# Kernel tuning notes

Measured on AMD Instinct MI355X. Metric: run time of the kernel, lower is better.

Reference implementation:

```python
import jax, jax.numpy as jnp
import numpy as np

B, C, O, H, W = 16, 256, 256, 64, 64
T_DIM, E, K = 512, 4, 3


def setup_inputs() -> dict:
    key = jax.random.key(0)
    ks = jax.random.split(key, 12)
    def rn(k, shape, s=0.02):
        return jax.random.normal(k, shape, jnp.float32) * s
    return dict(
        x=jax.random.normal(ks[0], (B, C, H, W), jnp.float32),
        time_emb=jax.random.normal(ks[1], (B, T_DIM), jnp.float32),
        Wq=rn(ks[2], (C, T_DIM)), bq=jnp.zeros((C,), jnp.float32),
        Wk=rn(ks[3], (C, C)), bk=jnp.zeros((C,), jnp.float32),
        Wv=rn(ks[4], (C, C)), bv=jnp.zeros((C,), jnp.float32),
        Wm1=rn(ks[5], (C // 4, C)), bm1=jnp.zeros((C // 4,), jnp.float32),
        Wm2=rn(ks[6], (C, C // 4)), bm2=jnp.zeros((C,), jnp.float32),
        Wc=rn(ks[7], (E, C)), bc=jnp.zeros((E,), jnp.float32),
        expert_w=rn(ks[8], (E, O, C, K, K), s=0.05),  # [E, O, C_in/groups, K, K]
        expert_b=rn(ks[9], (E, O), s=0.05),
    )


def reference(x, time_emb, Wq, bq, Wk, bk, Wv, bv, Wm1, bm1, Wm2, bm2, Wc, bc, expert_w, expert_b):
    # --- router (eval mode: no gating noise) ---
    pooled = x.mean(axis=(2, 3))                      # [B, C] == avg_pool over full HxW
    q = time_emb @ Wq.T + bq                          # [B, C]
    k = pooled @ Wk.T + bk                            # [B, C]
    attn = jax.nn.sigmoid(q * k)
    v = pooled @ Wv.T + bv
    x_att = v * attn
    h = jax.nn.gelu(x_att @ Wm1.T + bm1, approximate=False) @ Wm2.T + bm2
    x_mix = x_att + h
    logits = x_mix @ Wc.T + bc                        # [B, E]
    rw = jnp.tanh(logits)                             # routing weights [B, E]

    # --- per-sample expert-weight mixing ---
    w_eff = jnp.einsum('be,eoihw->boihw', rw, expert_w)  # [B, O, C, K, K]
    b_eff = rw @ expert_b                                 # [B, O]

    # --- per-sample conv (equivalent to groups=B trick) ---
    def conv_one(xb, wb):
        # xb: [C, H, W], wb: [O, C, K, K]
        return jax.lax.conv_general_dilated(
            xb[None], wb, window_strides=(1, 1), padding=[(1, 1), (1, 1)],
            dimension_numbers=('NCHW', 'OIHW', 'NCHW'))[0]

    out = jax.vmap(conv_one)(x, w_eff)                 # [B, O, H, W]
    return out + b_eff[:, :, None, None]
```

## Files before the change

### kernel.cpp

```cpp
#include <hip/hip_runtime.h>

typedef __bf16 bf16x8 __attribute__((ext_vector_type(8)));
typedef float f32x4 __attribute__((ext_vector_type(4)));

__device__ __forceinline__ unsigned short f2bf(float f) {
  union { float f; unsigned int u; } v;
  v.f = f;
  unsigned int r = v.u + 0x7FFFu + ((v.u >> 16) & 1u);
  return (unsigned short)(r >> 16);
}

__device__ __forceinline__ void load_lds16(const void* g, void* l) {
  __builtin_amdgcn_global_load_lds(
      (__attribute__((address_space(1))) void*)(void*)g,
      (__attribute__((address_space(3))) void*)l, 16, 0, 0);
}

__global__ void transpose_kernel(const float* __restrict__ x, unsigned short* __restrict__ xTpad,
                                 float* __restrict__ part) {
  int bid = blockIdx.x;
  int b = bid / 66, hp = bid % 66;
  unsigned short* rowbase = xTpad + ((size_t)(b * 66 + hp)) * 66 * 256;
  int t = threadIdx.x;
  if (hp == 0 || hp == 65) {
    uint4 z = make_uint4(0u, 0u, 0u, 0u);
    for (int i = t; i < 2112; i += 256) ((uint4*)rowbase)[i] = z;
    return;
  }
  int h = hp - 1;
  __shared__ unsigned short lds[64][264];
  __shared__ float psum[256];
  const float* xb = x + ((size_t)b * 256 * 64 + h) * 64;
  int lane = t & 63;
  #pragma unroll
  for (int g = 0; g < 16; ++g) {
    int c = g * 16 + (t >> 4);
    int w0 = (t & 15) * 4;
    float4 v = *(const float4*)&xb[(size_t)c * 4096 + w0];
    lds[w0 + 0][c] = f2bf(v.x);
    lds[w0 + 1][c] = f2bf(v.y);
    lds[w0 + 2][c] = f2bf(v.z);
    lds[w0 + 3][c] = f2bf(v.w);
    float s = v.x + v.y + v.z + v.w;
    s += __shfl_xor(s, 1); s += __shfl_xor(s, 2);
    s += __shfl_xor(s, 4); s += __shfl_xor(s, 8);
    if ((lane & 15) == 0) psum[c] = s;
  }
  __syncthreads();
  #pragma unroll
  for (int p = 0; p < 8; ++p) {
    int w = p * 8 + (t >> 5);
    int seg = t & 31;
    uint4 u = *(const uint4*)&lds[w][seg * 8];
    *(uint4*)&rowbase[(w + 1) * 256 + seg * 8] = u;
  }
  if (t < 64) {
    uint4 z = make_uint4(0u, 0u, 0u, 0u);
    int row = (t >> 5) ? 65 : 0;
    *(uint4*)&rowbase[row * 256 + (t & 31) * 8] = z;
  }
  if (t < 256) part[((size_t)b * 64 + h) * 256 + t] = psum[t];
}

__global__ void router_kernel(
    const float* __restrict__ time_emb, const float* __restrict__ part,
    const float* __restrict__ Wq, const float* __restrict__ bq,
    const float* __restrict__ Wk, const float* __restrict__ bk,
    const float* __restrict__ Wv, const float* __restrict__ bv,
    const float* __restrict__ Wm1, const float* __restrict__ bm1,
    const float* __restrict__ Wm2, const float* __restrict__ bm2,
    const float* __restrict__ Wc, const float* __restrict__ bc,
    const float* __restrict__ expert_b,
    float* __restrict__ rw_out, float* __restrict__ beff_out) {
  int b = blockIdx.x, tid = threadIdx.x;
  int t = tid & 255;
  __shared__ float te[512], pl[256], qs[256], xa[256], m1s[64], xms[256], rws[4];
  te[tid] = time_emb[b * 512 + tid];
  if (tid < 256) {
    float s = 0.f;
    const float* pp = part + (size_t)b * 16384 + tid;
    for (int hh = 0; hh < 64; ++hh) s += pp[hh * 256];
    pl[tid] = s * (1.0f / 4096.0f);
  }
  __syncthreads();
  if (tid < 256) {
    float q = bq[t];
    const float4* wq4 = (const float4*)(Wq + (size_t)t * 512);
    #pragma unroll 4
    for (int i = 0; i < 128; ++i) {
      float4 w4 = wq4[i];
      q += w4.x * te[i*4] + w4.y * te[i*4+1] + w4.z * te[i*4+2] + w4.w * te[i*4+3];
    }
    qs[t] = q;
  } else {
    float k = bk[t], v = bv[t];
    const float4* wk4 = (const float4*)(Wk + (size_t)t * 256);
    const float4* wv4 = (const float4*)(Wv + (size_t)t * 256);
    #pragma unroll 4
    for (int i = 0; i < 64; ++i) {
      float4 a4 = wk4[i], b4 = wv4[i];
      float p0 = pl[i*4], p1 = pl[i*4+1], p2 = pl[i*4+2], p3 = pl[i*4+3];
      k += a4.x * p0 + a4.y * p1 + a4.z * p2 + a4.w * p3;
      v += b4.x * p0 + b4.y * p1 + b4.z * p2 + b4.w * p3;
    }
    xa[t] = k;
    xms[t] = v;
  }
  __syncthreads();
  if (tid < 256) {
    float k = xa[t], v = xms[t];
    float attn = 1.0f / (1.0f + expf(-(qs[t] * k)));
    float xatt = v * attn;
    qs[t] = xatt;
  }
  __syncthreads();
  if (tid < 64) {
    float s = bm1[tid];
    const float4* w1 = (const float4*)(Wm1 + (size_t)tid * 256);
    #pragma unroll 4
    for (int i = 0; i < 64; ++i) {
      float4 w4 = w1[i];
      s += w4.x * qs[i*4] + w4.y * qs[i*4+1] + w4.z * qs[i*4+2] + w4.w * qs[i*4+3];
    }
    m1s[tid] = 0.5f * s * (1.0f + erff(s * 0.7071067811865476f));
  }
  __syncthreads();
  if (tid < 256) {
    float hsum = bm2[t];
    const float* w2 = Wm2 + (size_t)t * 64;
    for (int j = 0; j < 64; ++j) hsum += m1s[j] * w2[j];
    xms[t] = qs[t] + hsum;
  }
  __syncthreads();
  if (tid < 4) {
    float s = bc[tid];
    const float* wc = Wc + (size_t)tid * 256;
    for (int i = 0; i < 256; ++i) s += xms[i] * wc[i];
    float r = tanhf(s);
    rws[tid] = r;
    rw_out[b * 4 + tid] = r;
  }
  __syncthreads();
  if (tid < 256) {
    float be = 0.f;
    #pragma unroll
    for (int e = 0; e < 4; ++e) be += rws[e] * expert_b[e * 256 + t];
    beff_out[b * 256 + t] = be;
  }
}

__global__ void wmix_kernel(const float* __restrict__ ew, const float* __restrict__ rw,
                            unsigned short* __restrict__ wmix) {
  int o = blockIdx.x, t = threadIdx.x;
  __shared__ float lew[4][2304];
  __shared__ float rsh[64];
  if (t < 64) rsh[t] = rw[t];
  #pragma unroll
  for (int e = 0; e < 4; ++e) {
    const float* s = ew + ((size_t)e * 256 + o) * 2304;
    #pragma unroll
    for (int j = 0; j < 9; ++j) lew[e][j * 256 + t] = s[j * 256 + t];
  }
  __syncthreads();
  float wv[4][9];
  #pragma unroll
  for (int e = 0; e < 4; ++e)
    #pragma unroll
    for (int tt = 0; tt < 9; ++tt) wv[e][tt] = lew[e][t * 9 + tt];
  for (int b = 0; b < 16; ++b) {
    float r0 = rsh[b*4], r1 = rsh[b*4+1], r2 = rsh[b*4+2], r3 = rsh[b*4+3];
    unsigned short* wo = wmix + ((size_t)b * 256 + o) * 2304 + t;
    #pragma unroll
    for (int tt = 0; tt < 9; ++tt) {
      float m = r0 * wv[0][tt] + r1 * wv[1][tt] + r2 * wv[2][tt] + r3 * wv[3][tt];
      wo[tt * 256] = f2bf(m);
    }
  }
}

__global__ __launch_bounds__(512, 2) void conv_kernel(
    const unsigned short* __restrict__ xT, const unsigned short* __restrict__ wmix,
    const float* __restrict__ beff, float* __restrict__ out) {
  __shared__ unsigned short As[2][16384];
  __shared__ unsigned short Bs[2][16384];
  int bid = blockIdx.x;
  int b = ((bid & 7) << 1) | ((bid >> 7) & 1);
  int nt = (bid >> 3) & 15;
  int h0 = nt << 2;
  int tid = threadIdx.x;
  int wid = tid >> 6, lane = tid & 63;
  int lm = lane & 15, lg = lane >> 4;
  int wm = wid >> 1, wn = wid & 1;

  const unsigned short* wmb = wmix + (size_t)b * 256 * 2304;
  const unsigned short* xTb = xT + (size_t)b * 66 * 66 * 256;

  int lr = lane >> 3;
  int slot_g = (lane & 7) ^ lr;
  int a_lane = lr * 2304 + slot_g * 8;
  int b_lane = lr * 256 + slot_g * 8;

  int sw0 = ((0 + lg) ^ (lm & 7)) * 8;
  int sw1 = ((4 + lg) ^ (lm & 7)) * 8;

  auto stA = [&](int buf, int s, int u) {
    const unsigned short* src = wmb + (size_t)(u * 64 + wid * 8) * 2304 + s * 64 + a_lane;
    load_lds16(src, &As[buf][(u * 64 + wid * 8) * 64]);
  };
  auto stB = [&](int buf, int s, int bh, int rq) {
    int tap = s >> 2;
    int kh = tap / 3, kw = tap - kh * 3;
    int c0 = (s & 3) * 64;
    const unsigned short* src =
        xTb + (size_t)((h0 + bh * 2 + rq + kh) * 66 + wid * 8 + kw) * 256 + c0 + b_lane;
    load_lds16(src, &Bs[buf][(bh * 128 + rq * 64 + wid * 8) * 64]);
  };

  f32x4 acc[4][8];
  #pragma unroll
  for (int mf = 0; mf < 4; ++mf)
    #pragma unroll
    for (int nf = 0; nf < 8; ++nf)
      acc[mf][nf] = (f32x4){0.f, 0.f, 0.f, 0.f};

  stA(0, 0, 0); stA(0, 0, 1); stA(0, 0, 2); stA(0, 0, 3);
  stB(0, 0, 0, 0); stB(0, 0, 1, 0);
  stB(0, 0, 0, 1); stB(0, 0, 1, 1);
  asm volatile("s_waitcnt vmcnt(2)" ::: "memory");
  __builtin_amdgcn_s_barrier();

  auto do_tile = [&](int t, int BUF) __attribute__((always_inline)) {
    bool st = (t < 35);
    int s = t + 1;
    bf16x8 a01[2][2], a23[2][2], bA[4][2], bB[4][2];
    #pragma unroll
    for (int mf = 0; mf < 2; ++mf) {
      a01[mf][0] = *(const bf16x8*)&As[BUF][(wm * 64 + mf * 16 + lm) * 64 + sw0];
      a01[mf][1] = *(const bf16x8*)&As[BUF][(wm * 64 + mf * 16 + lm) * 64 + sw1];
    }
    #pragma unroll
    for (int nf = 0; nf < 4; ++nf) {
      bA[nf][0] = *(const bf16x8*)&Bs[BUF][(wn * 128 + nf * 16 + lm) * 64 + sw0];
      bA[nf][1] = *(const bf16x8*)&Bs[BUF][(wn * 128 + nf * 16 + lm) * 64 + sw1];
    }
    if (st) {
      stA(BUF ^ 1, s, 0); stA(BUF ^ 1, s, 1); stA(BUF ^ 1, s, 2); stA(BUF ^ 1, s, 3);
      stB(BUF ^ 1, s, 0, 0); stB(BUF ^ 1, s, 1, 0);
      stB(BUF ^ 1, s, 0, 1); stB(BUF ^ 1, s, 1, 1);
    }
    __builtin_amdgcn_s_barrier();
    asm volatile("s_waitcnt lgkmcnt(0)" ::: "memory");
    __builtin_amdgcn_sched_barrier(0);
    __builtin_amdgcn_s_setprio(1);
    #pragma unroll
    for (int mf = 0; mf < 2; ++mf)
      #pragma unroll
      for (int nf = 0; nf < 4; ++nf)
        #pragma unroll
        for (int kk = 0; kk < 2; ++kk)
          acc[mf][nf] = __builtin_amdgcn_mfma_f32_16x16x32_bf16(a01[mf][kk], bA[nf][kk], acc[mf][nf], 0, 0, 0);
    __builtin_amdgcn_s_setprio(0);
    __builtin_amdgcn_s_barrier();
    #pragma unroll
    for (int mf = 0; mf < 2; ++mf) {
      a23[mf][0] = *(const bf16x8*)&As[BUF][(wm * 64 + (mf + 2) * 16 + lm) * 64 + sw0];
      a23[mf][1] = *(const bf16x8*)&As[BUF][(wm * 64 + (mf + 2) * 16 + lm) * 64 + sw1];
    }
    if (st) { asm volatile("s_waitcnt vmcnt(8)" ::: "memory"); }
    else    { asm volatile("s_waitcnt vmcnt(0)" ::: "memory"); }
    __builtin_amdgcn_s_barrier();
    asm volatile("s_waitcnt lgkmcnt(0)" ::: "memory");
    __builtin_amdgcn_sched_barrier(0);
    __builtin_amdgcn_s_setprio(1);
    #pragma unroll
    for (int mf = 0; mf < 2; ++mf)
      #pragma unroll
      for (int nf = 0; nf < 4; ++nf)
        #pragma unroll
        for (int kk = 0; kk < 2; ++kk)
          acc[mf + 2][nf] = __builtin_amdgcn_mfma_f32_16x16x32_bf16(a23[mf][kk], bA[nf][kk], acc[mf + 2][nf], 0, 0, 0);
    __builtin_amdgcn_s_setprio(0);
    __builtin_amdgcn_s_barrier();
    #pragma unroll
    for (int nf = 0; nf < 4; ++nf) {
      bB[nf][0] = *(const bf16x8*)&Bs[BUF][(wn * 128 + 64 + nf * 16 + lm) * 64 + sw0];
      bB[nf][1] = *(const bf16x8*)&Bs[BUF][(wn * 128 + 64 + nf * 16 + lm) * 64 + sw1];
    }
    __builtin_amdgcn_s_barrier();
    asm volatile("s_waitcnt lgkmcnt(0)" ::: "memory");
    __builtin_amdgcn_sched_barrier(0);
    __builtin_amdgcn_s_setprio(1);
    #pragma unroll
    for (int mf = 0; mf < 2; ++mf)
      #pragma unroll
      for (int nf = 0; nf < 4; ++nf)
        #pragma unroll
        for (int kk = 0; kk < 2; ++kk)
          acc[mf + 2][nf + 4] = __builtin_amdgcn_mfma_f32_16x16x32_bf16(a23[mf][kk], bB[nf][kk], acc[mf + 2][nf + 4], 0, 0, 0);
    __builtin_amdgcn_s_setprio(0);
    __builtin_amdgcn_s_barrier();
    __builtin_amdgcn_s_setprio(1);
    #pragma unroll
    for (int mf = 0; mf < 2; ++mf)
      #pragma unroll
      for (int nf = 0; nf < 4; ++nf)
        #pragma unroll
        for (int kk = 0; kk < 2; ++kk)
          acc[mf][nf + 4] = __builtin_amdgcn_mfma_f32_16x16x32_bf16(a01[mf][kk], bB[nf][kk], acc[mf][nf + 4], 0, 0, 0);
    __builtin_amdgcn_s_setprio(0);
    if (st) { asm volatile("s_waitcnt vmcnt(2)" ::: "memory"); }
    else    { asm volatile("s_waitcnt vmcnt(0)" ::: "memory"); }
    __builtin_amdgcn_s_barrier();
  };

  for (int th = 0; th < 18; ++th) {
    do_tile(2 * th, 0);
    do_tile(2 * th + 1, 1);
  }

  #pragma unroll
  for (int mf = 0; mf < 4; ++mf) {
    int o = wm * 64 + mf * 16 + lg * 4;
    float be0 = beff[b * 256 + o + 0];
    float be1 = beff[b * 256 + o + 1];
    float be2 = beff[b * 256 + o + 2];
    float be3 = beff[b * 256 + o + 3];
    #pragma unroll
    for (int nf = 0; nf < 8; ++nf) {
      int n = wn * 128 + nf * 16 + lm;
      int hh = h0 + (n >> 6), w = n & 63;
      float* op = out + (((size_t)(b * 256 + o)) * 64 + hh) * 64 + w;
      op[0]            = acc[mf][nf][0] + be0;
      op[4096]         = acc[mf][nf][1] + be1;
      op[2 * 4096]     = acc[mf][nf][2] + be2;
      op[3 * 4096]     = acc[mf][nf][3] + be3;
    }
  }
}

extern "C" void kernel_launch(void* const* d_in, const int* in_sizes, int n_in,
                              void* d_out, int out_size, void* d_ws, size_t ws_size,
                              hipStream_t stream) {
  const float* x        = (const float*)d_in[0];
  const float* time_emb = (const float*)d_in[1];
  const float* Wq = (const float*)d_in[2];
  const float* bq = (const float*)d_in[3];
  const float* Wk = (const float*)d_in[4];
  const float* bk = (const float*)d_in[5];
  const float* Wv = (const float*)d_in[6];
  const float* bv = (const float*)d_in[7];
  const float* Wm1 = (const float*)d_in[8];
  const float* bm1 = (const float*)d_in[9];
  const float* Wm2 = (const float*)d_in[10];
  const float* bm2 = (const float*)d_in[11];
  const float* Wc = (const float*)d_in[12];
  const float* bc = (const float*)d_in[13];
  const float* expert_w = (const float*)d_in[14];
  const float* expert_b = (const float*)d_in[15];
  float* out = (float*)d_out;

  char* ws = (char*)d_ws;
  float* rw   = (float*)(ws + 0);
  float* beff = (float*)(ws + 1024);
  float* part = (float*)(ws + 20480);
  unsigned short* xTpad = (unsigned short*)(ws + 1069056);
  unsigned short* wmix  = (unsigned short*)(ws + 1069056 + 35684352);

  transpose_kernel<<<1056, 256, 0, stream>>>(x, xTpad, part);
  router_kernel<<<16, 512, 0, stream>>>(time_emb, part, Wq, bq, Wk, bk, Wv, bv,
                                        Wm1, bm1, Wm2, bm2, Wc, bc, expert_b, rw, beff);
  wmix_kernel<<<256, 256, 0, stream>>>(expert_w, rw, wmix);
  conv_kernel<<<256, 512, 0, stream>>>(xTpad, wmix, beff, out);
}
```

Baseline: 152.6 us.

## Split conv LDS into quarter slots and stagger loads across MFMA phases

```diff
diff --git a/kernel.cpp b/kernel.cpp
--- a/kernel.cpp
+++ b/kernel.cpp
@@ -110,8 +110,7 @@
   if (tid < 256) {
     float k = xa[t], v = xms[t];
     float attn = 1.0f / (1.0f + expf(-(qs[t] * k)));
-    float xatt = v * attn;
-    qs[t] = xatt;
+    qs[t] = v * attn;
   }
   __syncthreads();
   if (tid < 64) {
@@ -181,8 +180,8 @@
 __global__ __launch_bounds__(512, 2) void conv_kernel(
     const unsigned short* __restrict__ xT, const unsigned short* __restrict__ wmix,
     const float* __restrict__ beff, float* __restrict__ out) {
-  __shared__ unsigned short As[2][16384];
-  __shared__ unsigned short Bs[2][16384];
+  __shared__ unsigned short As[4][8192];
+  __shared__ unsigned short Bs[4][8192];
   int bid = blockIdx.x;
   int b = ((bid & 7) << 1) | ((bid >> 7) & 1);
   int nt = (bid >> 3) & 15;
@@ -203,17 +202,15 @@
   int sw0 = ((0 + lg) ^ (lm & 7)) * 8;
   int sw1 = ((4 + lg) ^ (lm & 7)) * 8;
 
-  auto stA = [&](int buf, int s, int u) {
-    const unsigned short* src = wmb + (size_t)(u * 64 + wid * 8) * 2304 + s * 64 + a_lane;
-    load_lds16(src, &As[buf][(u * 64 + wid * 8) * 64]);
+  auto stA = [&](int slot, int kh, int cc, int kw, int u) {
+    const unsigned short* src =
+        wmb + (size_t)(u * 64 + wid * 8) * 2304 + (kh * 3 + kw) * 256 + cc * 64 + a_lane;
+    load_lds16(src, &As[slot][((u & 1) * 64 + wid * 8) * 64]);
   };
-  auto stB = [&](int buf, int s, int bh, int rq) {
-    int tap = s >> 2;
-    int kh = tap / 3, kw = tap - kh * 3;
-    int c0 = (s & 3) * 64;
+  auto stB = [&](int slot, int kh, int cc, int kw, int hg) {
     const unsigned short* src =
-        xTb + (size_t)((h0 + bh * 2 + rq + kh) * 66 + wid * 8 + kw) * 256 + c0 + b_lane;
-    load_lds16(src, &Bs[buf][(bh * 128 + rq * 64 + wid * 8) * 64]);
+        xTb + (size_t)((h0 + hg + kh) * 66 + wid * 8 + kw) * 256 + cc * 64 + b_lane;
+    load_lds16(src, &Bs[slot][((hg & 1) * 64 + wid * 8) * 64]);
   };
 
   f32x4 acc[4][8];
@@ -223,99 +220,182 @@
     for (int nf = 0; nf < 8; ++nf)
       acc[mf][nf] = (f32x4){0.f, 0.f, 0.f, 0.f};
 
-  stA(0, 0, 0); stA(0, 0, 1); stA(0, 0, 2); stA(0, 0, 3);
-  stB(0, 0, 0, 0); stB(0, 0, 1, 0);
-  stB(0, 0, 0, 1); stB(0, 0, 1, 1);
-  asm volatile("s_waitcnt vmcnt(2)" ::: "memory");
+  const int arow = (wm & 1) * 64;
+  const int aslot = wm >> 1;
+  const int bslot = wn;
+
+  stA(0, 0, 0, 0, 0); stA(0, 0, 0, 0, 1); stA(1, 0, 0, 0, 2); stA(1, 0, 0, 0, 3);
+  stB(0, 0, 0, 0, 0); stB(0, 0, 0, 0, 1); stB(1, 0, 0, 0, 2); stB(1, 0, 0, 0, 3);
+  stA(2, 0, 0, 1, 0); stA(2, 0, 0, 1, 1); stA(3, 0, 0, 1, 2); stA(3, 0, 0, 1, 3);
+  stB(2, 0, 0, 1, 0); stB(2, 0, 0, 1, 1); stB(3, 0, 0, 1, 2); stB(3, 0, 0, 1, 3);
+  asm volatile("s_waitcnt vmcnt(8)" ::: "memory");
   __builtin_amdgcn_s_barrier();
 
-  auto do_tile = [&](int t, int BUF) __attribute__((always_inline)) {
-    bool st = (t < 35);
-    int s = t + 1;
+  for (int i = 0; i < 18; ++i) {
+    bool st = (i < 17);
+    int ta = 2 * i + 2, tb = 2 * i + 3;
+    int kha = ta / 12, ra = ta % 12;
+    int cca = ra / 3,  kwa = ra % 3;
+    int khb = tb / 12, rb = tb % 12;
+    int ccb = rb / 3,  kwb = rb % 3;
+
     bf16x8 a01[2][2], a23[2][2], bA[4][2], bB[4][2];
+
     #pragma unroll
     for (int mf = 0; mf < 2; ++mf) {
-      a01[mf][0] = *(const bf16x8*)&As[BUF][(wm * 64 + mf * 16 + lm) * 64 + sw0];
-      a01[mf][1] = *(const bf16x8*)&As[BUF][(wm * 64 + mf * 16 + lm) * 64 + sw1];
+      a01[mf][0] = *(const bf16x8*)&As[aslot][(arow + mf * 16 + lm) * 64 + sw0];
+      a01[mf][1] = *(const bf16x8*)&As[aslot][(arow + mf * 16 + lm) * 64 + sw1];
     }
     #pragma unroll
     for (int nf = 0; nf < 4; ++nf) {
-      bA[nf][0] = *(const bf16x8*)&Bs[BUF][(wn * 128 + nf * 16 + lm) * 64 + sw0];
-      bA[nf][1] = *(const bf16x8*)&Bs[BUF][(wn * 128 + nf * 16 + lm) * 64 + sw1];
+      bA[nf][0] = *(const bf16x8*)&Bs[bslot][(nf * 16 + lm) * 64 + sw0];
+      bA[nf][1] = *(const bf16x8*)&Bs[bslot][(nf * 16 + lm) * 64 + sw1];
+    }
+    __builtin_amdgcn_s_barrier();
+    asm volatile("s_waitcnt lgkmcnt(0)" ::: "memory");
+    __builtin_amdgcn_sched_barrier(0);
+    __builtin_amdgcn_s_setprio(1);
+    #pragma unroll
+    for (int mf = 0; mf < 2; ++mf)
+      #pragma unroll
+      for (int nf = 0; nf < 4; ++nf)
+        #pragma unroll
+        for (int kk = 0; kk < 2; ++kk)
+          acc[mf][nf] = __builtin_amdgcn_mfma_f32_16x16x32_bf16(a01[mf][kk], bA[nf][kk], acc[mf][nf], 0, 0, 0);
+    __builtin_amdgcn_s_setprio(0);
+    __builtin_amdgcn_s_barrier();
+    #pragma unroll
+    for (int mf = 0; mf < 2; ++mf) {
+      a23[mf][0] = *(const bf16x8*)&As[aslot][(arow + (mf + 2) * 16 + lm) * 64 + sw0];
+      a23[mf][1] = *(const bf16x8*)&As[aslot][(arow + (mf + 2) * 16 + lm) * 64 + sw1];
+    }
+    __builtin_amdgcn_s_barrier();
+    asm volatile("s_waitcnt lgkmcnt(0)" ::: "memory");
+    __builtin_amdgcn_sched_barrier(0);
+    __builtin_amdgcn_s_setprio(1);
+    #pragma unroll
+    for (int mf = 0; mf < 2; ++mf)
+      #pragma unroll
+      for (int nf = 0; nf < 4; ++nf)
+        #pragma unroll
+        for (int kk = 0; kk < 2; ++kk)
+          acc[mf + 2][nf] = __builtin_amdgcn_mfma_f32_16x16x32_bf16(a23[mf][kk], bA[nf][kk], acc[mf + 2][nf], 0, 0, 0);
+    __builtin_amdgcn_s_setprio(0);
+    __builtin_amdgcn_s_barrier();
+    #pragma unroll
+    for (int nf = 0; nf < 4; ++nf) {
+      bB[nf][0] = *(const bf16x8*)&Bs[bslot][(64 + nf * 16 + lm) * 64 + sw0];
+      bB[nf][1] = *(const bf16x8*)&Bs[bslot][(64 + nf * 16 + lm) * 64 + sw1];
+    }
+    if (st) { stA(0, kha, cca, kwa, 0); stA(0, kha, cca, kwa, 1); }
+    __builtin_amdgcn_s_barrier();
+    asm volatile("s_waitcnt lgkmcnt(0)" ::: "memory");
+    __builtin_amdgcn_sched_barrier(0);
+    __builtin_amdgcn_s_setprio(1);
+    #pragma unroll
+    for (int mf = 0; mf < 2; ++mf)
+      #pragma unroll
+      for (int nf = 0; nf < 4; ++nf)
+        #pragma unroll
+        for (int kk = 0; kk < 2; ++kk)
+          acc[mf + 2][nf + 4] = __builtin_amdgcn_mfma_f32_16x16x32_bf16(a23[mf][kk], bB[nf][kk], acc[mf + 2][nf + 4], 0, 0, 0);
+    __builtin_amdgcn_s_setprio(0);
+    __builtin_amdgcn_s_barrier();
+    if (st) { stA(1, kha, cca, kwa, 2); stA(1, kha, cca, kwa, 3); }
+    __builtin_amdgcn_s_setprio(1);
+    #pragma unroll
+    for (int mf = 0; mf < 2; ++mf)
+      #pragma unroll
+      for (int nf = 0; nf < 4; ++nf)
+        #pragma unroll
+        for (int kk = 0; kk < 2; ++kk)
+          acc[mf][nf + 4] = __builtin_amdgcn_mfma_f32_16x16x32_bf16(a01[mf][kk], bB[nf][kk], acc[mf][nf + 4], 0, 0, 0);
+    __builtin_amdgcn_s_setprio(0);
+    if (st) { asm volatile("s_waitcnt vmcnt(4)" ::: "memory"); }
+    else    { asm volatile("s_waitcnt vmcnt(0)" ::: "memory"); }
+    __builtin_amdgcn_s_barrier();
+
+    #pragma unroll
+    for (int mf = 0; mf < 2; ++mf) {
+      a01[mf][0] = *(const bf16x8*)&As[aslot + 2][(arow + mf * 16 + lm) * 64 + sw0];
+      a01[mf][1] = *(const bf16x8*)&As[aslot + 2][(arow + mf * 16 + lm) * 64 + sw1];
+    }
+    #pragma unroll
+    for (int nf = 0; nf < 4; ++nf) {
+      bA[nf][0] = *(const bf16x8*)&Bs[bslot + 2][(nf * 16 + lm) * 64 + sw0];
+      bA[nf][1] = *(const bf16x8*)&Bs[bslot + 2][(nf * 16 + lm) * 64 + sw1];
+    }
+    if (st) { stB(0, kha, cca, kwa, 0); stB(0, kha, cca, kwa, 1); }
+    __builtin_amdgcn_s_barrier();
+    asm volatile("s_waitcnt lgkmcnt(0)" ::: "memory");
+    __builtin_amdgcn_sched_barrier(0);
+    __builtin_amdgcn_s_setprio(1);
+    #pragma unroll
+    for (int mf = 0; mf < 2; ++mf)
+      #pragma unroll
+      for (int nf = 0; nf < 4; ++nf)
+        #pragma unroll
+        for (int kk = 0; kk < 2; ++kk)
+          acc[mf][nf] = __builtin_amdgcn_mfma_f32_16x16x32_bf16(a01[mf][kk], bA[nf][kk], acc[mf][nf], 0, 0, 0);
+    __builtin_amdgcn_s_setprio(0);
+    __builtin_amdgcn_s_barrier();
+    #pragma unroll
+    for (int mf = 0; mf < 2; ++mf) {
+      a23[mf][0] = *(const bf16x8*)&As[aslot + 2][(arow + (mf + 2) * 16 + lm) * 64 + sw0];
+      a23[mf][1] = *(const bf16x8*)&As[aslot + 2][(arow + (mf + 2) * 16 + lm) * 64 + sw1];
+    }
+    if (st) { stB(1, kha, cca, kwa, 2); stB(1, kha, cca, kwa, 3); }
+    __builtin_amdgcn_s_barrier();
+    asm volatile("s_waitcnt lgkmcnt(0)" ::: "memory");
+    __builtin_amdgcn_sched_barrier(0);
+    __builtin_amdgcn_s_setprio(1);
+    #pragma unroll
+    for (int mf = 0; mf < 2; ++mf)
+      #pragma unroll
+      for (int nf = 0; nf < 4; ++nf)
+        #pragma unroll
+        for (int kk = 0; kk < 2; ++kk)
+          acc[mf + 2][nf] = __builtin_amdgcn_mfma_f32_16x16x32_bf16(a23[mf][kk], bA[nf][kk], acc[mf + 2][nf], 0, 0, 0);
+    __builtin_amdgcn_s_setprio(0);
+    __builtin_amdgcn_s_barrier();
+    #pragma unroll
+    for (int nf = 0; nf < 4; ++nf) {
+      bB[nf][0] = *(const bf16x8*)&Bs[bslot + 2][(64 + nf * 16 + lm) * 64 + sw0];
+      bB[nf][1] = *(const bf16x8*)&Bs[bslot + 2][(64 + nf * 16 + lm) * 64 + sw1];
     }
     if (st) {
-      stA(BUF ^ 1, s, 0); stA(BUF ^ 1, s, 1); stA(BUF ^ 1, s, 2); stA(BUF ^ 1, s, 3);
-      stB(BUF ^ 1, s, 0, 0); stB(BUF ^ 1, s, 1, 0);
-      stB(BUF ^ 1, s, 0, 1); stB(BUF ^ 1, s, 1, 1);
-    }
-    __builtin_amdgcn_s_barrier();
-    asm volatile("s_waitcnt lgkmcnt(0)" ::: "memory");
-    __builtin_amdgcn_sched_barrier(0);
-    __builtin_amdgcn_s_setprio(1);
-    #pragma unroll
-    for (int mf = 0; mf < 2; ++mf)
-      #pragma unroll
-      for (int nf = 0; nf < 4; ++nf)
-        #pragma unroll
-        for (int kk = 0; kk < 2; ++kk)
-          acc[mf][nf] = __builtin_amdgcn_mfma_f32_16x16x32_bf16(a01[mf][kk], bA[nf][kk], acc[mf][nf], 0, 0, 0);
-    __builtin_amdgcn_s_setprio(0);
-    __builtin_amdgcn_s_barrier();
-    #pragma unroll
-    for (int mf = 0; mf < 2; ++mf) {
-      a23[mf][0] = *(const bf16x8*)&As[BUF][(wm * 64 + (mf + 2) * 16 + lm) * 64 + sw0];
-      a23[mf][1] = *(const bf16x8*)&As[BUF][(wm * 64 + (mf + 2) * 16 + lm) * 64 + sw1];
-    }
+      stA(2, khb, ccb, kwb, 0); stA(2, khb, ccb, kwb, 1);
+      stA(3, khb, ccb, kwb, 2); stA(3, khb, ccb, kwb, 3);
+    }
+    __builtin_amdgcn_s_barrier();
+    asm volatile("s_waitcnt lgkmcnt(0)" ::: "memory");
+    __builtin_amdgcn_sched_barrier(0);
+    __builtin_amdgcn_s_setprio(1);
+    #pragma unroll
+    for (int mf = 0; mf < 2; ++mf)
+      #pragma unroll
+      for (int nf = 0; nf < 4; ++nf)
+        #pragma unroll
+        for (int kk = 0; kk < 2; ++kk)
+          acc[mf + 2][nf + 4] = __builtin_amdgcn_mfma_f32_16x16x32_bf16(a23[mf][kk], bB[nf][kk], acc[mf + 2][nf + 4], 0, 0, 0);
+    __builtin_amdgcn_s_setprio(0);
+    __builtin_amdgcn_s_barrier();
+    if (st) {
+      stB(2, khb, ccb, kwb, 0); stB(2, khb, ccb, kwb, 1);
+      stB(3, khb, ccb, kwb, 2); stB(3, khb, ccb, kwb, 3);
+    }
+    __builtin_amdgcn_s_setprio(1);
+    #pragma unroll
+    for (int mf = 0; mf < 2; ++mf)
+      #pragma unroll
+      for (int nf = 0; nf < 4; ++nf)
+        #pragma unroll
+        for (int kk = 0; kk < 2; ++kk)
+          acc[mf][nf + 4] = __builtin_amdgcn_mfma_f32_16x16x32_bf16(a01[mf][kk], bB[nf][kk], acc[mf][nf + 4], 0, 0, 0);
+    __builtin_amdgcn_s_setprio(0);
     if (st) { asm volatile("s_waitcnt vmcnt(8)" ::: "memory"); }
     else    { asm volatile("s_waitcnt vmcnt(0)" ::: "memory"); }
     __builtin_amdgcn_s_barrier();
-    asm volatile("s_waitcnt lgkmcnt(0)" ::: "memory");
-    __builtin_amdgcn_sched_barrier(0);
-    __builtin_amdgcn_s_setprio(1);
-    #pragma unroll
-    for (int mf = 0; mf < 2; ++mf)
-      #pragma unroll
-      for (int nf = 0; nf < 4; ++nf)
-        #pragma unroll
-        for (int kk = 0; kk < 2; ++kk)
-          acc[mf + 2][nf] = __builtin_amdgcn_mfma_f32_16x16x32_bf16(a23[mf][kk], bA[nf][kk], acc[mf + 2][nf], 0, 0, 0);
-    __builtin_amdgcn_s_setprio(0);
-    __builtin_amdgcn_s_barrier();
-    #pragma unroll
-    for (int nf = 0; nf < 4; ++nf) {
-      bB[nf][0] = *(const bf16x8*)&Bs[BUF][(wn * 128 + 64 + nf * 16 + lm) * 64 + sw0];
-      bB[nf][1] = *(const bf16x8*)&Bs[BUF][(wn * 128 + 64 + nf * 16 + lm) * 64 + sw1];
-    }
-    __builtin_amdgcn_s_barrier();
-    asm volatile("s_waitcnt lgkmcnt(0)" ::: "memory");
-    __builtin_amdgcn_sched_barrier(0);
-    __builtin_amdgcn_s_setprio(1);
-    #pragma unroll
-    for (int mf = 0; mf < 2; ++mf)
-      #pragma unroll
-      for (int nf = 0; nf < 4; ++nf)
-        #pragma unroll
-        for (int kk = 0; kk < 2; ++kk)
-          acc[mf + 2][nf + 4] = __builtin_amdgcn_mfma_f32_16x16x32_bf16(a23[mf][kk], bB[nf][kk], acc[mf + 2][nf + 4], 0, 0, 0);
-    __builtin_amdgcn_s_setprio(0);
-    __builtin_amdgcn_s_barrier();
-    __builtin_amdgcn_s_setprio(1);
-    #pragma unroll
-    for (int mf = 0; mf < 2; ++mf)
-      #pragma unroll
-      for (int nf = 0; nf < 4; ++nf)
-        #pragma unroll
-        for (int kk = 0; kk < 2; ++kk)
-          acc[mf][nf + 4] = __builtin_amdgcn_mfma_f32_16x16x32_bf16(a01[mf][kk], bB[nf][kk], acc[mf][nf + 4], 0, 0, 0);
-    __builtin_amdgcn_s_setprio(0);
-    if (st) { asm volatile("s_waitcnt vmcnt(2)" ::: "memory"); }
-    else    { asm volatile("s_waitcnt vmcnt(0)" ::: "memory"); }
-    __builtin_amdgcn_s_barrier();
-  };
-
-  for (int th = 0; th < 18; ++th) {
-    do_tile(2 * th, 0);
-    do_tile(2 * th + 1, 1);
   }
 
   #pragma unroll
```

Result: faster. 145.7 us (-4.5%).

## Restructure conv pipeline to two-tile-ahead prefetch with fewer barriers; rework transpose

Applied to the files above, without the earlier changes.

```diff
diff --git a/kernel.cpp b/kernel.cpp
--- a/kernel.cpp
+++ b/kernel.cpp
@@ -28,31 +28,32 @@
     return;
   }
   int h = hp - 1;
-  __shared__ unsigned short lds[64][264];
+  __shared__ float tile[64][65];
   __shared__ float psum[256];
   const float* xb = x + ((size_t)b * 256 * 64 + h) * 64;
-  int lane = t & 63;
-  #pragma unroll
-  for (int g = 0; g < 16; ++g) {
-    int c = g * 16 + (t >> 4);
-    int w0 = (t & 15) * 4;
-    float4 v = *(const float4*)&xb[(size_t)c * 4096 + w0];
-    lds[w0 + 0][c] = f2bf(v.x);
-    lds[w0 + 1][c] = f2bf(v.y);
-    lds[w0 + 2][c] = f2bf(v.z);
-    lds[w0 + 3][c] = f2bf(v.w);
-    float s = v.x + v.y + v.z + v.w;
-    s += __shfl_xor(s, 1); s += __shfl_xor(s, 2);
-    s += __shfl_xor(s, 4); s += __shfl_xor(s, 8);
-    if ((lane & 15) == 0) psum[c] = s;
-  }
-  __syncthreads();
-  #pragma unroll
-  for (int p = 0; p < 8; ++p) {
-    int w = p * 8 + (t >> 5);
-    int seg = t & 31;
-    uint4 u = *(const uint4*)&lds[w][seg * 8];
-    *(uint4*)&rowbase[(w + 1) * 256 + seg * 8] = u;
+  for (int sub = 0; sub < 4; ++sub) {
+    int c0 = sub * 64;
+    if (sub) __syncthreads();
+    #pragma unroll
+    for (int k = 0; k < 16; ++k) {
+      int cr = k * 4 + (t >> 6);
+      int w = t & 63;
+      float v = xb[(size_t)(c0 + cr) * 4096 + w];
+      tile[cr][w] = v;
+      float s = v;
+      s += __shfl_xor(s, 1);  s += __shfl_xor(s, 2);  s += __shfl_xor(s, 4);
+      s += __shfl_xor(s, 8);  s += __shfl_xor(s, 16); s += __shfl_xor(s, 32);
+      if ((t & 63) == 0) psum[c0 + cr] = s;
+    }
+    __syncthreads();
+    #pragma unroll
+    for (int p = 0; p < 8; ++p) {
+      int w = p * 8 + (t >> 5);
+      int cp = (t & 31) * 2;
+      float f0 = tile[cp][w], f1 = tile[cp + 1][w];
+      unsigned int u = (unsigned int)f2bf(f0) | ((unsigned int)f2bf(f1) << 16);
+      *(unsigned int*)&rowbase[(w + 1) * 256 + c0 + cp] = u;
+    }
   }
   if (t < 64) {
     uint4 z = make_uint4(0u, 0u, 0u, 0u);
@@ -110,8 +111,7 @@
   if (tid < 256) {
     float k = xa[t], v = xms[t];
     float attn = 1.0f / (1.0f + expf(-(qs[t] * k)));
-    float xatt = v * attn;
-    qs[t] = xatt;
+    qs[t] = v * attn;
   }
   __syncthreads();
   if (tid < 64) {
@@ -181,8 +181,8 @@
 __global__ __launch_bounds__(512, 2) void conv_kernel(
     const unsigned short* __restrict__ xT, const unsigned short* __restrict__ wmix,
     const float* __restrict__ beff, float* __restrict__ out) {
-  __shared__ unsigned short As[2][16384];
-  __shared__ unsigned short Bs[2][16384];
+  __shared__ unsigned short As[4][8192];
+  __shared__ unsigned short Bs[4][8192];
   int bid = blockIdx.x;
   int b = ((bid & 7) << 1) | ((bid >> 7) & 1);
   int nt = (bid >> 3) & 15;
@@ -203,17 +203,23 @@
   int sw0 = ((0 + lg) ^ (lm & 7)) * 8;
   int sw1 = ((4 + lg) ^ (lm & 7)) * 8;
 
-  auto stA = [&](int buf, int s, int u) {
-    const unsigned short* src = wmb + (size_t)(u * 64 + wid * 8) * 2304 + s * 64 + a_lane;
-    load_lds16(src, &As[buf][(u * 64 + wid * 8) * 64]);
-  };
-  auto stB = [&](int buf, int s, int bh, int rq) {
-    int tap = s >> 2;
-    int kh = tap / 3, kw = tap - kh * 3;
-    int c0 = (s & 3) * 64;
+  auto stA = [&](int slot, int kh, int cc, int kw, int u) {
     const unsigned short* src =
-        xTb + (size_t)((h0 + bh * 2 + rq + kh) * 66 + wid * 8 + kw) * 256 + c0 + b_lane;
-    load_lds16(src, &Bs[buf][(bh * 128 + rq * 64 + wid * 8) * 64]);
+        wmb + (size_t)(u * 64 + wid * 8) * 2304 + (kh * 3 + kw) * 256 + cc * 64 + a_lane;
+    load_lds16(src, &As[slot][((u & 1) * 64 + wid * 8) * 64]);
+  };
+  auto stB = [&](int slot, int kh, int cc, int kw, int hg) {
+    const unsigned short* src =
+        xTb + (size_t)((h0 + hg + kh) * 66 + wid * 8 + kw) * 256 + cc * 64 + b_lane;
+    load_lds16(src, &Bs[slot][((hg & 1) * 64 + wid * 8) * 64]);
+  };
+  auto stage_tile = [&](int t2) {
+    int kh = t2 / 12, r = t2 % 12, cc = r / 3, kw = r % 3;
+    int p2 = (t2 & 1) * 2;
+    stA(p2, kh, cc, kw, 0); stA(p2, kh, cc, kw, 1);
+    stA(p2 + 1, kh, cc, kw, 2); stA(p2 + 1, kh, cc, kw, 3);
+    stB(p2, kh, cc, kw, 0); stB(p2, kh, cc, kw, 1);
+    stB(p2 + 1, kh, cc, kw, 2); stB(p2 + 1, kh, cc, kw, 3);
   };
 
   f32x4 acc[4][8];
@@ -223,35 +229,22 @@
     for (int nf = 0; nf < 8; ++nf)
       acc[mf][nf] = (f32x4){0.f, 0.f, 0.f, 0.f};
 
-  stA(0, 0, 0); stA(0, 0, 1); stA(0, 0, 2); stA(0, 0, 3);
-  stB(0, 0, 0, 0); stB(0, 0, 1, 0);
-  stB(0, 0, 0, 1); stB(0, 0, 1, 1);
-  asm volatile("s_waitcnt vmcnt(2)" ::: "memory");
-  __builtin_amdgcn_s_barrier();
-
-  auto do_tile = [&](int t, int BUF) __attribute__((always_inline)) {
-    bool st = (t < 35);
-    int s = t + 1;
+  const int arow = (wm & 1) * 64;
+
+  auto region = [&](int p2) __attribute__((always_inline)) {
+    const int as0 = p2 + (wm >> 1);
+    const int bs0 = p2 + wn;
     bf16x8 a01[2][2], a23[2][2], bA[4][2], bB[4][2];
     #pragma unroll
     for (int mf = 0; mf < 2; ++mf) {
-      a01[mf][0] = *(const bf16x8*)&As[BUF][(wm * 64 + mf * 16 + lm) * 64 + sw0];
-      a01[mf][1] = *(const bf16x8*)&As[BUF][(wm * 64 + mf * 16 + lm) * 64 + sw1];
+      a01[mf][0] = *(const bf16x8*)&As[as0][(arow + mf * 16 + lm) * 64 + sw0];
+      a01[mf][1] = *(const bf16x8*)&As[as0][(arow + mf * 16 + lm) * 64 + sw1];
     }
     #pragma unroll
     for (int nf = 0; nf < 4; ++nf) {
-      bA[nf][0] = *(const bf16x8*)&Bs[BUF][(wn * 128 + nf * 16 + lm) * 64 + sw0];
-      bA[nf][1] = *(const bf16x8*)&Bs[BUF][(wn * 128 + nf * 16 + lm) * 64 + sw1];
-    }
-    if (st) {
-      stA(BUF ^ 1, s, 0); stA(BUF ^ 1, s, 1); stA(BUF ^ 1, s, 2); stA(BUF ^ 1, s, 3);
-      stB(BUF ^ 1, s, 0, 0); stB(BUF ^ 1, s, 1, 0);
-      stB(BUF ^ 1, s, 0, 1); stB(BUF ^ 1, s, 1, 1);
-    }
-    __builtin_amdgcn_s_barrier();
-    asm volatile("s_waitcnt lgkmcnt(0)" ::: "memory");
-    __builtin_amdgcn_sched_barrier(0);
-    __builtin_amdgcn_s_setprio(1);
+      bA[nf][0] = *(const bf16x8*)&Bs[bs0][(nf * 16 + lm) * 64 + sw0];
+      bA[nf][1] = *(const bf16x8*)&Bs[bs0][(nf * 16 + lm) * 64 + sw1];
+    }
     #pragma unroll
     for (int mf = 0; mf < 2; ++mf)
       #pragma unroll
@@ -259,19 +252,11 @@
         #pragma unroll
         for (int kk = 0; kk < 2; ++kk)
           acc[mf][nf] = __builtin_amdgcn_mfma_f32_16x16x32_bf16(a01[mf][kk], bA[nf][kk], acc[mf][nf], 0, 0, 0);
-    __builtin_amdgcn_s_setprio(0);
-    __builtin_amdgcn_s_barrier();
     #pragma unroll
     for (int mf = 0; mf < 2; ++mf) {
-      a23[mf][0] = *(const bf16x8*)&As[BUF][(wm * 64 + (mf + 2) * 16 + lm) * 64 + sw0];
-      a23[mf][1] = *(const bf16x8*)&As[BUF][(wm * 64 + (mf + 2) * 16 + lm) * 64 + sw1];
-    }
-    if (st) { asm volatile("s_waitcnt vmcnt(8)" ::: "memory"); }
-    else    { asm volatile("s_waitcnt vmcnt(0)" ::: "memory"); }
-    __builtin_amdgcn_s_barrier();
-    asm volatile("s_waitcnt lgkmcnt(0)" ::: "memory");
-    __builtin_amdgcn_sched_barrier(0);
-    __builtin_amdgcn_s_setprio(1);
+      a23[mf][0] = *(const bf16x8*)&As[as0][(arow + (mf + 2) * 16 + lm) * 64 + sw0];
+      a23[mf][1] = *(const bf16x8*)&As[as0][(arow + (mf + 2) * 16 + lm) * 64 + sw1];
+    }
     #pragma unroll
     for (int mf = 0; mf < 2; ++mf)
       #pragma unroll
@@ -279,17 +264,11 @@
         #pragma unroll
         for (int kk = 0; kk < 2; ++kk)
           acc[mf + 2][nf] = __builtin_amdgcn_mfma_f32_16x16x32_bf16(a23[mf][kk], bA[nf][kk], acc[mf + 2][nf], 0, 0, 0);
-    __builtin_amdgcn_s_setprio(0);
-    __builtin_amdgcn_s_barrier();
     #pragma unroll
     for (int nf = 0; nf < 4; ++nf) {
-      bB[nf][0] = *(const bf16x8*)&Bs[BUF][(wn * 128 + 64 + nf * 16 + lm) * 64 + sw0];
-      bB[nf][1] = *(const bf16x8*)&Bs[BUF][(wn * 128 + 64 + nf * 16 + lm) * 64 + sw1];
-    }
-    __builtin_amdgcn_s_barrier();
-    asm volatile("s_waitcnt lgkmcnt(0)" ::: "memory");
-    __builtin_amdgcn_sched_barrier(0);
-    __builtin_amdgcn_s_setprio(1);
+      bB[nf][0] = *(const bf16x8*)&Bs[bs0][(64 + nf * 16 + lm) * 64 + sw0];
+      bB[nf][1] = *(const bf16x8*)&Bs[bs0][(64 + nf * 16 + lm) * 64 + sw1];
+    }
     #pragma unroll
     for (int mf = 0; mf < 2; ++mf)
       #pragma unroll
@@ -297,9 +276,6 @@
         #pragma unroll
         for (int kk = 0; kk < 2; ++kk)
           acc[mf + 2][nf + 4] = __builtin_amdgcn_mfma_f32_16x16x32_bf16(a23[mf][kk], bB[nf][kk], acc[mf + 2][nf + 4], 0, 0, 0);
-    __builtin_amdgcn_s_setprio(0);
-    __builtin_amdgcn_s_barrier();
-    __builtin_amdgcn_s_setprio(1);
     #pragma unroll
     for (int mf = 0; mf < 2; ++mf)
       #pragma unroll
@@ -307,15 +283,30 @@
         #pragma unroll
         for (int kk = 0; kk < 2; ++kk)
           acc[mf][nf + 4] = __builtin_amdgcn_mfma_f32_16x16x32_bf16(a01[mf][kk], bB[nf][kk], acc[mf][nf + 4], 0, 0, 0);
-    __builtin_amdgcn_s_setprio(0);
-    if (st) { asm volatile("s_waitcnt vmcnt(2)" ::: "memory"); }
-    else    { asm volatile("s_waitcnt vmcnt(0)" ::: "memory"); }
+  };
+
+  auto tail = [&](int t) __attribute__((always_inline)) {
+    __builtin_amdgcn_sched_barrier(0);
     __builtin_amdgcn_s_barrier();
-  };
-
-  for (int th = 0; th < 18; ++th) {
-    do_tile(2 * th, 0);
-    do_tile(2 * th + 1, 1);
+    if (t < 34) {
+      stage_tile(t + 2);
+      asm volatile("s_waitcnt vmcnt(8)" ::: "memory");
+    } else {
+      asm volatile("s_waitcnt vmcnt(0)" ::: "memory");
+    }
+    __builtin_amdgcn_s_barrier();
+  };
+
+  stage_tile(0);
+  stage_tile(1);
+  asm volatile("s_waitcnt vmcnt(8)" ::: "memory");
+  __builtin_amdgcn_s_barrier();
+
+  for (int i = 0; i < 18; ++i) {
+    region(0);
+    tail(2 * i);
+    region(2);
+    if (i < 17) tail(2 * i + 1);
   }
 
   #pragma unroll
```

Result: slower. 169.2 us (+10.8%).

## Pre-swizzle mixed weights into MFMA fragment layout and load A directly to registers

Applied to the files above, without the earlier changes.

```diff
diff --git a/kernel.cpp b/kernel.cpp
--- a/kernel.cpp
+++ b/kernel.cpp
@@ -110,8 +110,7 @@
   if (tid < 256) {
     float k = xa[t], v = xms[t];
     float attn = 1.0f / (1.0f + expf(-(qs[t] * k)));
-    float xatt = v * attn;
-    qs[t] = xatt;
+    qs[t] = v * attn;
   }
   __syncthreads();
   if (tid < 64) {
@@ -150,38 +149,39 @@
 }
 
 __global__ void wmix_kernel(const float* __restrict__ ew, const float* __restrict__ rw,
-                            unsigned short* __restrict__ wmix) {
-  int o = blockIdx.x, t = threadIdx.x;
-  __shared__ float lew[4][2304];
+                            unsigned short* __restrict__ wmixT) {
+  int ob = blockIdx.x % 16, kr = blockIdx.x / 16;
+  int t = threadIdx.x;
+  int lm = t & 15, kcl = t >> 4;
+  int kc = kr * 16 + kcl;
+  int tap = kc >> 5;
+  int c0 = (kc & 31) * 8;
   __shared__ float rsh[64];
   if (t < 64) rsh[t] = rw[t];
+  int o = ob * 16 + lm;
+  float wv[4][8];
   #pragma unroll
   for (int e = 0; e < 4; ++e) {
-    const float* s = ew + ((size_t)e * 256 + o) * 2304;
-    #pragma unroll
-    for (int j = 0; j < 9; ++j) lew[e][j * 256 + t] = s[j * 256 + t];
-  }
-  __syncthreads();
-  float wv[4][9];
-  #pragma unroll
-  for (int e = 0; e < 4; ++e)
-    #pragma unroll
-    for (int tt = 0; tt < 9; ++tt) wv[e][tt] = lew[e][t * 9 + tt];
+    const float* s = ew + (((size_t)e * 256 + o) * 256 + c0) * 9 + tap;
+    #pragma unroll
+    for (int j = 0; j < 8; ++j) wv[e][j] = s[j * 9];
+  }
+  __syncthreads();
   for (int b = 0; b < 16; ++b) {
     float r0 = rsh[b*4], r1 = rsh[b*4+1], r2 = rsh[b*4+2], r3 = rsh[b*4+3];
-    unsigned short* wo = wmix + ((size_t)b * 256 + o) * 2304 + t;
-    #pragma unroll
-    for (int tt = 0; tt < 9; ++tt) {
-      float m = r0 * wv[0][tt] + r1 * wv[1][tt] + r2 * wv[2][tt] + r3 * wv[3][tt];
-      wo[tt * 256] = f2bf(m);
-    }
+    unsigned short tmp[8];
+    #pragma unroll
+    for (int j = 0; j < 8; ++j) {
+      float m = r0*wv[0][j] + r1*wv[1][j] + r2*wv[2][j] + r3*wv[3][j];
+      tmp[j] = f2bf(m);
+    }
+    *(uint4*)&wmixT[(((size_t)(b*16 + ob)*288 + kc)*128) + lm*8] = *(uint4*)tmp;
   }
 }
 
 __global__ __launch_bounds__(512, 2) void conv_kernel(
-    const unsigned short* __restrict__ xT, const unsigned short* __restrict__ wmix,
+    const unsigned short* __restrict__ xT, const unsigned short* __restrict__ wmixT,
     const float* __restrict__ beff, float* __restrict__ out) {
-  __shared__ unsigned short As[2][16384];
   __shared__ unsigned short Bs[2][16384];
   int bid = blockIdx.x;
   int b = ((bid & 7) << 1) | ((bid >> 7) & 1);
@@ -192,28 +192,20 @@
   int lm = lane & 15, lg = lane >> 4;
   int wm = wid >> 1, wn = wid & 1;
 
-  const unsigned short* wmb = wmix + (size_t)b * 256 * 2304;
   const unsigned short* xTb = xT + (size_t)b * 66 * 66 * 256;
+  const unsigned short* wmA = wmixT + (size_t)(b * 16 + wm * 4) * 288 * 128 + lane * 8;
 
   int lr = lane >> 3;
   int slot_g = (lane & 7) ^ lr;
-  int a_lane = lr * 2304 + slot_g * 8;
   int b_lane = lr * 256 + slot_g * 8;
 
   int sw0 = ((0 + lg) ^ (lm & 7)) * 8;
   int sw1 = ((4 + lg) ^ (lm & 7)) * 8;
 
-  auto stA = [&](int buf, int s, int u) {
-    const unsigned short* src = wmb + (size_t)(u * 64 + wid * 8) * 2304 + s * 64 + a_lane;
-    load_lds16(src, &As[buf][(u * 64 + wid * 8) * 64]);
-  };
-  auto stB = [&](int buf, int s, int bh, int rq) {
-    int tap = s >> 2;
-    int kh = tap / 3, kw = tap - kh * 3;
-    int c0 = (s & 3) * 64;
+  auto stB = [&](int buf, int kh, int cc, int kw, int q) {
     const unsigned short* src =
-        xTb + (size_t)((h0 + bh * 2 + rq + kh) * 66 + wid * 8 + kw) * 256 + c0 + b_lane;
-    load_lds16(src, &Bs[buf][(bh * 128 + rq * 64 + wid * 8) * 64]);
+        xTb + (size_t)((h0 + q + kh) * 66 + wid * 8 + kw) * 256 + cc * 64 + b_lane;
+    load_lds16(src, &Bs[buf][(q * 64 + wid * 8) * 64]);
   };
 
   f32x4 acc[4][8];
@@ -223,99 +215,53 @@
     for (int nf = 0; nf < 8; ++nf)
       acc[mf][nf] = (f32x4){0.f, 0.f, 0.f, 0.f};
 
-  stA(0, 0, 0); stA(0, 0, 1); stA(0, 0, 2); stA(0, 0, 3);
-  stB(0, 0, 0, 0); stB(0, 0, 1, 0);
-  stB(0, 0, 0, 1); stB(0, 0, 1, 1);
-  asm volatile("s_waitcnt vmcnt(2)" ::: "memory");
+  bf16x8 Ae[4][2], Ao[4][2];
+
+  stB(0, 0, 0, 0, 0); stB(0, 0, 0, 0, 1); stB(0, 0, 0, 0, 2); stB(0, 0, 0, 0, 3);
+  __builtin_amdgcn_sched_barrier(0);
+  #pragma unroll
+  for (int mf = 0; mf < 4; ++mf)
+    #pragma unroll
+    for (int kk = 0; kk < 2; ++kk)
+      Ae[mf][kk] = *(const bf16x8*)(wmA + (size_t)(mf * 288 + kk * 4) * 128);
+  asm volatile("s_waitcnt vmcnt(8)" ::: "memory");
   __builtin_amdgcn_s_barrier();
 
-  auto do_tile = [&](int t, int BUF) __attribute__((always_inline)) {
+  auto tile_body = [&](int t, int buf, bf16x8 (&Acur)[4][2], bf16x8 (&Anext)[4][2])
+      __attribute__((always_inline)) {
     bool st = (t < 35);
-    int s = t + 1;
-    bf16x8 a01[2][2], a23[2][2], bA[4][2], bB[4][2];
-    #pragma unroll
-    for (int mf = 0; mf < 2; ++mf) {
-      a01[mf][0] = *(const bf16x8*)&As[BUF][(wm * 64 + mf * 16 + lm) * 64 + sw0];
-      a01[mf][1] = *(const bf16x8*)&As[BUF][(wm * 64 + mf * 16 + lm) * 64 + sw1];
-    }
-    #pragma unroll
-    for (int nf = 0; nf < 4; ++nf) {
-      bA[nf][0] = *(const bf16x8*)&Bs[BUF][(wn * 128 + nf * 16 + lm) * 64 + sw0];
-      bA[nf][1] = *(const bf16x8*)&Bs[BUF][(wn * 128 + nf * 16 + lm) * 64 + sw1];
-    }
     if (st) {
-      stA(BUF ^ 1, s, 0); stA(BUF ^ 1, s, 1); stA(BUF ^ 1, s, 2); stA(BUF ^ 1, s, 3);
-      stB(BUF ^ 1, s, 0, 0); stB(BUF ^ 1, s, 1, 0);
-      stB(BUF ^ 1, s, 0, 1); stB(BUF ^ 1, s, 1, 1);
-    }
-    __builtin_amdgcn_s_barrier();
-    asm volatile("s_waitcnt lgkmcnt(0)" ::: "memory");
-    __builtin_amdgcn_sched_barrier(0);
-    __builtin_amdgcn_s_setprio(1);
-    #pragma unroll
-    for (int mf = 0; mf < 2; ++mf)
+      int tn = t + 1;
+      int khn = tn / 12, rn = tn % 12, ccn = rn / 3, kwn = rn % 3;
+      stB(buf ^ 1, khn, ccn, kwn, 0); stB(buf ^ 1, khn, ccn, kwn, 1);
+      stB(buf ^ 1, khn, ccn, kwn, 2); stB(buf ^ 1, khn, ccn, kwn, 3);
+      __builtin_amdgcn_sched_barrier(0);
+      int kbase = (khn * 3 + kwn) * 32 + ccn * 8;
       #pragma unroll
-      for (int nf = 0; nf < 4; ++nf)
+      for (int mf = 0; mf < 4; ++mf)
         #pragma unroll
         for (int kk = 0; kk < 2; ++kk)
-          acc[mf][nf] = __builtin_amdgcn_mfma_f32_16x16x32_bf16(a01[mf][kk], bA[nf][kk], acc[mf][nf], 0, 0, 0);
-    __builtin_amdgcn_s_setprio(0);
-    __builtin_amdgcn_s_barrier();
-    #pragma unroll
-    for (int mf = 0; mf < 2; ++mf) {
-      a23[mf][0] = *(const bf16x8*)&As[BUF][(wm * 64 + (mf + 2) * 16 + lm) * 64 + sw0];
-      a23[mf][1] = *(const bf16x8*)&As[BUF][(wm * 64 + (mf + 2) * 16 + lm) * 64 + sw1];
-    }
-    if (st) { asm volatile("s_waitcnt vmcnt(8)" ::: "memory"); }
-    else    { asm volatile("s_waitcnt vmcnt(0)" ::: "memory"); }
-    __builtin_amdgcn_s_barrier();
-    asm volatile("s_waitcnt lgkmcnt(0)" ::: "memory");
-    __builtin_amdgcn_sched_barrier(0);
-    __builtin_amdgcn_s_setprio(1);
-    #pragma unroll
-    for (int mf = 0; mf < 2; ++mf)
+          Anext[mf][kk] = *(const bf16x8*)(wmA + (size_t)(mf * 288 + kbase + kk * 4) * 128);
+    }
+    #pragma unroll
+    for (int nf = 0; nf < 8; ++nf) {
+      bf16x8 b0 = *(const bf16x8*)&Bs[buf][(wn * 128 + nf * 16 + lm) * 64 + sw0];
+      bf16x8 b1 = *(const bf16x8*)&Bs[buf][(wn * 128 + nf * 16 + lm) * 64 + sw1];
       #pragma unroll
-      for (int nf = 0; nf < 4; ++nf)
-        #pragma unroll
-        for (int kk = 0; kk < 2; ++kk)
-          acc[mf + 2][nf] = __builtin_amdgcn_mfma_f32_16x16x32_bf16(a23[mf][kk], bA[nf][kk], acc[mf + 2][nf], 0, 0, 0);
-    __builtin_amdgcn_s_setprio(0);
-    __builtin_amdgcn_s_barrier();
-    #pragma unroll
-    for (int nf = 0; nf < 4; ++nf) {
-      bB[nf][0] = *(const bf16x8*)&Bs[BUF][(wn * 128 + 64 + nf * 16 + lm) * 64 + sw0];
-      bB[nf][1] = *(const bf16x8*)&Bs[BUF][(wn * 128 + 64 + nf * 16 + lm) * 64 + sw1];
-    }
-    __builtin_amdgcn_s_barrier();
-    asm volatile("s_waitcnt lgkmcnt(0)" ::: "memory");
-    __builtin_amdgcn_sched_barrier(0);
-    __builtin_amdgcn_s_setprio(1);
-    #pragma unroll
-    for (int mf = 0; mf < 2; ++mf)
-      #pragma unroll
-      for (int nf = 0; nf < 4; ++nf)
-        #pragma unroll
-        for (int kk = 0; kk < 2; ++kk)
-          acc[mf + 2][nf + 4] = __builtin_amdgcn_mfma_f32_16x16x32_bf16(a23[mf][kk], bB[nf][kk], acc[mf + 2][nf + 4], 0, 0, 0);
-    __builtin_amdgcn_s_setprio(0);
-    __builtin_amdgcn_s_barrier();
-    __builtin_amdgcn_s_setprio(1);
-    #pragma unroll
-    for (int mf = 0; mf < 2; ++mf)
-      #pragma unroll
-      for (int nf = 0; nf < 4; ++nf)
-        #pragma unroll
-        for (int kk = 0; kk < 2; ++kk)
-          acc[mf][nf + 4] = __builtin_amdgcn_mfma_f32_16x16x32_bf16(a01[mf][kk], bB[nf][kk], acc[mf][nf + 4], 0, 0, 0);
-    __builtin_amdgcn_s_setprio(0);
-    if (st) { asm volatile("s_waitcnt vmcnt(2)" ::: "memory"); }
-    else    { asm volatile("s_waitcnt vmcnt(0)" ::: "memory"); }
-    __builtin_amdgcn_s_barrier();
+      for (int mf = 0; mf < 4; ++mf) {
+        acc[mf][nf] = __builtin_amdgcn_mfma_f32_16x16x32_bf16(Acur[mf][0], b0, acc[mf][nf], 0, 0, 0);
+        acc[mf][nf] = __builtin_amdgcn_mfma_f32_16x16x32_bf16(Acur[mf][1], b1, acc[mf][nf], 0, 0, 0);
+      }
+    }
+    if (st) {
+      asm volatile("s_waitcnt vmcnt(8)" ::: "memory");
+      __builtin_amdgcn_s_barrier();
+    }
   };
 
-  for (int th = 0; th < 18; ++th) {
-    do_tile(2 * th, 0);
-    do_tile(2 * th + 1, 1);
+  for (int i = 0; i < 18; ++i) {
+    tile_body(2 * i, 0, Ae, Ao);
+    tile_body(2 * i + 1, 1, Ao, Ae);
   }
 
   #pragma unroll
@@ -363,12 +309,12 @@
   float* rw   = (float*)(ws + 0);
   float* beff = (float*)(ws + 1024);
   float* part = (float*)(ws + 20480);
-  unsigned short* xTpad = (unsigned short*)(ws + 1069056);
-  unsigned short* wmix  = (unsigned short*)(ws + 1069056 + 35684352);
+  unsigned short* xTpad  = (unsigned short*)(ws + 1069056);
+  unsigned short* wmixT  = (unsigned short*)(ws + 1069056 + 35684352);
 
   transpose_kernel<<<1056, 256, 0, stream>>>(x, xTpad, part);
   router_kernel<<<16, 512, 0, stream>>>(time_emb, part, Wq, bq, Wk, bk, Wv, bv,
                                         Wm1, bm1, Wm2, bm2, Wc, bc, expert_b, rw, beff);
-  wmix_kernel<<<256, 256, 0, stream>>>(expert_w, rw, wmix);
-  conv_kernel<<<256, 512, 0, stream>>>(xTpad, wmix, beff, out);
-}
+  wmix_kernel<<<288, 256, 0, stream>>>(expert_w, rw, wmixT);
+  conv_kernel<<<256, 512, 0, stream>>>(xTpad, wmixT, beff, out);
+}
```

After: 162.6 us. 6.5% more time.
